# Performance work log

Hardware: AMD Instinct MI355X
Metric: run time of the kernel (lower is better)

Reference implementation:

```python
import jax, jax.numpy as jnp
import numpy as np

N_NODES = 50000
N_EDGES = 800000
DIM = 256


def setup_inputs() -> dict:
    key = jax.random.key(0)
    k1, k2, k3, k4 = jax.random.split(key, 4)
    x = jax.random.normal(k1, (N_NODES, DIM), dtype=jnp.float32)
    edge_index = jax.random.randint(k2, (2, N_EDGES), 0, N_NODES, dtype=jnp.int64)
    # GCNConv learned params (glorot-style weight, zero bias like PyG default init)
    W = jax.random.normal(k3, (DIM, DIM), dtype=jnp.float32) * (1.0 / np.sqrt(DIM))
    b = jnp.zeros((DIM,), dtype=jnp.float32)
    return {"x": x, "edge_index": edge_index, "W": W, "b": b}


def reference(x, edge_index, W, b):
    # GNNBlock forward (eval mode: dropout is identity; normalizer=Identity,
    # activation=ReLU, projection=Identity since in_dim==out_dim).
    n = x.shape[0]
    # --- GCNConv with self-loops and symmetric normalization ---
    loop = jnp.arange(n, dtype=edge_index.dtype)
    src = jnp.concatenate([edge_index[0], loop])  # [E+N]
    dst = jnp.concatenate([edge_index[1], loop])  # [E+N]
    ones = jnp.ones(src.shape[0], dtype=x.dtype)
    deg = jax.ops.segment_sum(ones, dst, num_segments=n)  # in-degree incl. self-loop
    dinv = jnp.where(deg > 0, jax.lax.rsqrt(deg), 0.0)
    norm = dinv[src] * dinv[dst]  # [E+N]
    h = x @ W  # transform first (in->out), then aggregate
    msg = h[src] * norm[:, None]  # gather + scale, [E+N, DIM]
    agg = jax.ops.segment_sum(msg, dst, num_segments=n) + b  # scatter-add
    # --- norm (Identity) -> activation (ReLU) -> residual -> dropout (eval) ---
    out = jax.nn.relu(agg) + x
    return out
```

## Files before the change

kernel.cpp:

```cpp
#include <hip/hip_runtime.h>

#define N_NODES 50000
#define DIM 256
#define NBUCK 196
#define BCAP 6144
#define CEDGES 2048
#define APAD 264
#define EPAD 260

typedef __attribute__((ext_vector_type(8))) short bf16x8;
typedef __attribute__((ext_vector_type(4))) float f32x4;
typedef __attribute__((ext_vector_type(2))) float f32x2;
union U16 { uint4 u; bf16x8 s; };

__device__ __forceinline__ unsigned short f2b(float f) {
    unsigned int u = __float_as_uint(f);
    return (unsigned short)((u + 0x7FFFu + ((u >> 16) & 1u)) >> 16);
}

__global__ __launch_bounds__(256) void coarse_kernel(const int* __restrict__ src,
                                                     const int* __restrict__ dst, int E,
                                                     int* __restrict__ bcur,
                                                     unsigned int* __restrict__ slab) {
    __shared__ int hist[NBUCK];
    __shared__ int scn[NBUCK];
    __shared__ int gbase[NBUCK];
    __shared__ int cur[NBUCK];
    __shared__ int s2[256];
    __shared__ unsigned int sorted[CEDGES];

    const int tid = threadIdx.x;
    const int e0 = blockIdx.x * CEDGES;
    const int nE = min(CEDGES, E - e0);

    if (tid < NBUCK) hist[tid] = 0;
    __syncthreads();

    unsigned int pk[8];
    #pragma unroll
    for (int i = 0; i < 8; ++i) {
        int idx = i * 256 + tid;
        pk[i] = 0xFFFFFFFFu;
        if (idx < nE) {
            unsigned int s = (unsigned int)src[e0 + idx];
            unsigned int d = (unsigned int)dst[e0 + idx];
            pk[i] = (d << 16) | s;
            atomicAdd(&hist[d >> 8], 1);
        }
    }
    __syncthreads();

    int v = (tid < NBUCK) ? hist[tid] : 0;
    s2[tid] = v;
    __syncthreads();
    for (int off = 1; off < 256; off <<= 1) {
        int t = (tid >= off) ? s2[tid - off] : 0;
        __syncthreads();
        s2[tid] += t;
        __syncthreads();
    }
    if (tid < NBUCK) {
        scn[tid] = s2[tid] - v;
        cur[tid] = 0;
        gbase[tid] = (v > 0) ? atomicAdd(&bcur[tid], v) : 0;
    }
    __syncthreads();

    #pragma unroll
    for (int i = 0; i < 8; ++i) {
        if (pk[i] != 0xFFFFFFFFu) {
            int bkt = pk[i] >> 24;
            int p = scn[bkt] + atomicAdd(&cur[bkt], 1);
            sorted[p] = pk[i];
        }
    }
    __syncthreads();

    for (int i = tid; i < nE; i += 256) {
        unsigned int p = sorted[i];
        int bkt = p >> 24;
        int gpos = gbase[bkt] + (i - scn[bkt]);
        if (gpos < BCAP) slab[(size_t)bkt * BCAP + gpos] = p;
    }
}

__global__ __launch_bounds__(256) void fine_kernel(const int* __restrict__ bcnt,
                                                   const unsigned int* __restrict__ slab,
                                                   int* __restrict__ offs,
                                                   int* __restrict__ deg,
                                                   float* __restrict__ dinv,
                                                   int* __restrict__ csr_src) {
    __shared__ int red[256];
    __shared__ int hist[256];
    __shared__ int scn[256];
    __shared__ unsigned int stage[BCAP];

    const int tid = threadIdx.x;
    const int g = blockIdx.x;

    red[tid] = (tid < g) ? min(bcnt[tid], BCAP) : 0;
    __syncthreads();
    for (int off = 128; off > 0; off >>= 1) {
        if (tid < off) red[tid] += red[tid + off];
        __syncthreads();
    }
    const int base = red[0];
    const int cnt = min(bcnt[g], BCAP);

    hist[tid] = 0;
    __syncthreads();
    for (int i = tid; i < cnt; i += 256) {
        unsigned int p = slab[(size_t)g * BCAP + i];
        stage[i] = p;
        atomicAdd(&hist[(p >> 16) & 255], 1);
    }
    __syncthreads();

    int d = hist[tid];
    scn[tid] = d;
    __syncthreads();
    for (int off = 1; off < 256; off <<= 1) {
        int t = (tid >= off) ? scn[tid - off] : 0;
        __syncthreads();
        scn[tid] += t;
        __syncthreads();
    }
    int excl = scn[tid] - d;

    int node = g * 256 + tid;
    if (node < N_NODES) {
        offs[node] = base + excl;
        deg[node]  = d;
        dinv[node] = rsqrtf((float)(d + 1));
    }
    hist[tid] = excl;
    __syncthreads();

    for (int i = tid; i < cnt; i += 256) {
        unsigned int p = stage[i];
        int pos = atomicAdd(&hist[(p >> 16) & 255], 1);
        csr_src[base + pos] = (int)(p & 0xFFFFu);
    }
}

__global__ __launch_bounds__(256) void prep_kernel(const float* __restrict__ W,
                                                   uint4* __restrict__ Bpack,
                                                   const float* __restrict__ x,
                                                   const float* __restrict__ dinv,
                                                   unsigned int* __restrict__ xq) {
    if (blockIdx.x < 32) {
        int gid  = blockIdx.x * 256 + threadIdx.x;
        int lane = gid & 63;
        int u    = (gid >> 6) & 15;
        int ki   = gid >> 10;
        int n    = u * 16 + (lane & 15);
        int k0   = ki * 32 + (lane >> 4) * 8;
        unsigned int w[4];
        #pragma unroll
        for (int p = 0; p < 4; ++p) {
            unsigned int lo = f2b(W[(size_t)(k0 + 2 * p) * DIM + n]);
            unsigned int hi = f2b(W[(size_t)(k0 + 2 * p + 1) * DIM + n]);
            w[p] = lo | (hi << 16);
        }
        Bpack[gid] = make_uint4(w[0], w[1], w[2], w[3]);
    } else {
        int gid = (blockIdx.x - 32) * 256 + threadIdx.x;
        int row = gid >> 6;
        float di = dinv[row];
        float4 v = ((const float4*)x)[gid];
        int p = __builtin_amdgcn_cvt_pk_fp8_f32(v.x * di, v.y * di, 0, false);
        p     = __builtin_amdgcn_cvt_pk_fp8_f32(v.z * di, v.w * di, p, true);
        xq[gid] = (unsigned int)p;
    }
}

__global__ __launch_bounds__(256) void agg_q_kernel(const unsigned int* __restrict__ xq,
                                                    const int* __restrict__ offs,
                                                    const int* __restrict__ deg,
                                                    const int* __restrict__ csr_src,
                                                    const float* __restrict__ dinv,
                                                    ushort4* __restrict__ aggb) {
    int row  = blockIdx.x * 4 + (threadIdx.x >> 6);
    int lane = threadIdx.x & 63;
    if (row >= N_NODES) return;

    float di = dinv[row];
    unsigned int qself = xq[(size_t)row * 64 + lane];
    f32x2 lo = __builtin_amdgcn_cvt_pk_f32_fp8((int)qself, false);
    f32x2 hi = __builtin_amdgcn_cvt_pk_f32_fp8((int)qself, true);
    float ax = lo.x, ay = lo.y, az = hi.x, aw = hi.y;

    int start = offs[row];
    int n     = deg[row];
    int i = 0;
    for (; i + 8 <= n; i += 8) {
        int s0 = csr_src[start + i + 0], s1 = csr_src[start + i + 1];
        int s2 = csr_src[start + i + 2], s3 = csr_src[start + i + 3];
        int s4 = csr_src[start + i + 4], s5 = csr_src[start + i + 5];
        int s6 = csr_src[start + i + 6], s7 = csr_src[start + i + 7];
        unsigned int q0 = xq[(size_t)s0 * 64 + lane];
        unsigned int q1 = xq[(size_t)s1 * 64 + lane];
        unsigned int q2 = xq[(size_t)s2 * 64 + lane];
        unsigned int q3 = xq[(size_t)s3 * 64 + lane];
        unsigned int q4 = xq[(size_t)s4 * 64 + lane];
        unsigned int q5 = xq[(size_t)s5 * 64 + lane];
        unsigned int q6 = xq[(size_t)s6 * 64 + lane];
        unsigned int q7 = xq[(size_t)s7 * 64 + lane];
        #pragma unroll
        for (int u = 0; u < 8; ++u) {
            unsigned int q;
            switch (u) {
                case 0: q = q0; break; case 1: q = q1; break;
                case 2: q = q2; break; case 3: q = q3; break;
                case 4: q = q4; break; case 5: q = q5; break;
                case 6: q = q6; break; default: q = q7; break;
            }
            f32x2 l = __builtin_amdgcn_cvt_pk_f32_fp8((int)q, false);
            f32x2 h = __builtin_amdgcn_cvt_pk_f32_fp8((int)q, true);
            ax += l.x; ay += l.y; az += h.x; aw += h.y;
        }
    }
    for (; i < n; ++i) {
        int s = csr_src[start + i];
        unsigned int q = xq[(size_t)s * 64 + lane];
        f32x2 l = __builtin_amdgcn_cvt_pk_f32_fp8((int)q, false);
        f32x2 h = __builtin_amdgcn_cvt_pk_f32_fp8((int)q, true);
        ax += l.x; ay += l.y; az += h.x; aw += h.y;
    }
    ax *= di; ay *= di; az *= di; aw *= di;
    aggb[(size_t)row * 64 + lane] = make_ushort4(f2b(ax), f2b(ay), f2b(az), f2b(aw));
}

__global__ __launch_bounds__(256) void gemm_kernel(const uint4* __restrict__ aggb16,
                                                   const float* __restrict__ x,
                                                   const uint4* __restrict__ Bpack,
                                                   const float* __restrict__ b,
                                                   float* __restrict__ out) {
    __shared__ __align__(16) char LDSraw[64 * APAD * 2];
    ushort* ALDS = (ushort*)LDSraw;
    float*  ELDS = (float*)LDSraw;

    const int tid  = threadIdx.x;
    const int row0 = blockIdx.x * 64;

    #pragma unroll
    for (int i = 0; i < 8; ++i) {
        int c = i * 256 + tid;
        int r = c >> 5;
        int q = c & 31;
        int row = row0 + r;
        uint4 v = make_uint4(0, 0, 0, 0);
        if (row < N_NODES) v = aggb16[(size_t)row * 32 + q];
        *(uint4*)&ALDS[r * APAD + q * 8] = v;
    }
    __syncthreads();

    const int wave = tid >> 6;
    const int lane = tid & 63;
    const int m    = lane & 15;
    const int kb   = lane >> 4;

    f32x4 acc[4][4];
    #pragma unroll
    for (int t = 0; t < 4; ++t)
        #pragma unroll
        for (int r = 0; r < 4; ++r) acc[t][r] = (f32x4){0.f, 0.f, 0.f, 0.f};

    const uint4* bp = Bpack + (size_t)(wave * 4) * 64 + lane;

    for (int ki = 0; ki < 8; ++ki) {
        U16 bf[4], af[4];
        #pragma unroll
        for (int t = 0; t < 4; ++t) bf[t].u = bp[(size_t)(ki * 16 + t) * 64];
        #pragma unroll
        for (int r = 0; r < 4; ++r)
            af[r].u = *(const uint4*)&ALDS[(r * 16 + m) * APAD + ki * 32 + kb * 8];
        #pragma unroll
        for (int t = 0; t < 4; ++t)
            #pragma unroll
            for (int r = 0; r < 4; ++r)
                acc[t][r] = __builtin_amdgcn_mfma_f32_16x16x32_bf16(af[r].s, bf[t].s, acc[t][r], 0, 0, 0);
    }

    const float4* x4g = (const float4*)x;
    const float4* b4  = (const float4*)b;
    float4* out4 = (float4*)out;

    #pragma unroll
    for (int p = 0; p < 2; ++p) {
        __syncthreads();
        #pragma unroll
        for (int t = 0; t < 4; ++t) {
            #pragma unroll
            for (int rl = 0; rl < 2; ++rl) {
                int r = p * 2 + rl;
                #pragma unroll
                for (int reg = 0; reg < 4; ++reg) {
                    ELDS[(rl * 16 + kb * 4 + reg) * EPAD + wave * 64 + t * 16 + m] = acc[t][r][reg];
                }
            }
        }
        __syncthreads();
        #pragma unroll
        for (int j = 0; j < 8; ++j) {
            int idx  = j * 256 + tid;
            int lrow = idx >> 6;
            int c4   = idx & 63;
            int grow = row0 + p * 32 + lrow;
            if (grow < N_NODES) {
                float4 v  = *(const float4*)&ELDS[lrow * EPAD + c4 * 4];
                float4 bb = b4[c4];
                float4 xx = x4g[(size_t)grow * 64 + c4];
                float4 o;
                o.x = fmaxf(v.x + bb.x, 0.f) + xx.x;
                o.y = fmaxf(v.y + bb.y, 0.f) + xx.y;
                o.z = fmaxf(v.z + bb.z, 0.f) + xx.z;
                o.w = fmaxf(v.w + bb.w, 0.f) + xx.w;
                out4[(size_t)grow * 64 + c4] = o;
            }
        }
    }
}

extern "C" void kernel_launch(void* const* d_in, const int* in_sizes, int n_in,
                              void* d_out, int out_size, void* d_ws, size_t ws_size,
                              hipStream_t stream) {
    const float* x  = (const float*)d_in[0];
    const int*   ei = (const int*)d_in[1];
    const float* W  = (const float*)d_in[2];
    const float* b  = (const float*)d_in[3];
    float* out = (float*)d_out;
    const int E = in_sizes[1] / 2;

    char* ws = (char*)d_ws;
    int*          bcur    = (int*)(ws);
    int*          deg     = (int*)(ws + 4096);
    int*          offs    = (int*)(ws + 208896);
    float*        dinv    = (float*)(ws + 413696);
    int*          csr_src = (int*)(ws + 618496);
    unsigned int* slab    = (unsigned int*)(ws + 3821568);
    ushort4*      aggb    = (ushort4*)(ws + 8640512);
    uint4*        Bpack   = (uint4*)(ws + 34240512);
    unsigned int* xq      = (unsigned int*)(ws + 34371584);

    const int* src = ei;
    const int* dst = ei + E;

    hipMemsetAsync(bcur, 0, NBUCK * sizeof(int), stream);

    coarse_kernel<<<(E + CEDGES - 1) / CEDGES, 256, 0, stream>>>(src, dst, E, bcur, slab);
    fine_kernel<<<NBUCK, 256, 0, stream>>>(bcur, slab, offs, deg, dinv, csr_src);
    prep_kernel<<<12532, 256, 0, stream>>>(W, Bpack, x, dinv, xq);
    agg_q_kernel<<<(N_NODES + 3) / 4, 256, 0, stream>>>(xq, offs, deg, csr_src, dinv, aggb);
    gemm_kernel<<<(N_NODES + 63) / 64, 256, 0, stream>>>((const uint4*)aggb, x, Bpack, b, out);
}
```

Baseline: 200.8 us.

## Replace two-pass bucket sort CSR build with cooperative atomic counting-sort kernel

Replaces the coarse/fine bucketed sort that built the CSR with a single cooperative kernel. It does a global atomic degree histogram, a grid-synced block scan for offsets, then scatters source indices through per-node atomic cursors. This removes one launch and the slab staging buffer. In exchange it adds three grid-wide syncs, heavy global atomic contention, and non-deterministic neighbour order within each node's list.

```diff
diff --git a/kernel.cpp b/kernel.cpp
--- a/kernel.cpp
+++ b/kernel.cpp
@@ -1,10 +1,12 @@
 #include <hip/hip_runtime.h>
+#include <hip/hip_cooperative_groups.h>
+
+namespace cg = cooperative_groups;
 
 #define N_NODES 50000
 #define DIM 256
-#define NBUCK 196
-#define BCAP 6144
-#define CEDGES 2048
+#define NBLK 256
+#define CHUNK 196
 #define APAD 264
 #define EPAD 260
 
@@ -18,106 +20,31 @@
     return (unsigned short)((u + 0x7FFFu + ((u >> 16) & 1u)) >> 16);
 }
 
-__global__ __launch_bounds__(256) void coarse_kernel(const int* __restrict__ src,
-                                                     const int* __restrict__ dst, int E,
-                                                     int* __restrict__ bcur,
-                                                     unsigned int* __restrict__ slab) {
-    __shared__ int hist[NBUCK];
-    __shared__ int scn[NBUCK];
-    __shared__ int gbase[NBUCK];
-    __shared__ int cur[NBUCK];
-    __shared__ int s2[256];
-    __shared__ unsigned int sorted[CEDGES];
+__global__ __launch_bounds__(256) void bin_kernel(const int* __restrict__ src,
+                                                  const int* __restrict__ dst, const int E,
+                                                  int* __restrict__ deg,
+                                                  int* __restrict__ offs,
+                                                  int* __restrict__ cursor,
+                                                  float* __restrict__ dinv,
+                                                  int* __restrict__ csr_src,
+                                                  int* __restrict__ bsum) {
+    cg::grid_group grid = cg::this_grid();
+    __shared__ int scn[256];
+    __shared__ int lexcl[256];
 
     const int tid = threadIdx.x;
-    const int e0 = blockIdx.x * CEDGES;
-    const int nE = min(CEDGES, E - e0);
-
-    if (tid < NBUCK) hist[tid] = 0;
-    __syncthreads();
-
-    unsigned int pk[8];
-    #pragma unroll
-    for (int i = 0; i < 8; ++i) {
-        int idx = i * 256 + tid;
-        pk[i] = 0xFFFFFFFFu;
-        if (idx < nE) {
-            unsigned int s = (unsigned int)src[e0 + idx];
-            unsigned int d = (unsigned int)dst[e0 + idx];
-            pk[i] = (d << 16) | s;
-            atomicAdd(&hist[d >> 8], 1);
-        }
-    }
-    __syncthreads();
-
-    int v = (tid < NBUCK) ? hist[tid] : 0;
-    s2[tid] = v;
-    __syncthreads();
-    for (int off = 1; off < 256; off <<= 1) {
-        int t = (tid >= off) ? s2[tid - off] : 0;
-        __syncthreads();
-        s2[tid] += t;
-        __syncthreads();
-    }
-    if (tid < NBUCK) {
-        scn[tid] = s2[tid] - v;
-        cur[tid] = 0;
-        gbase[tid] = (v > 0) ? atomicAdd(&bcur[tid], v) : 0;
-    }
-    __syncthreads();
-
-    #pragma unroll
-    for (int i = 0; i < 8; ++i) {
-        if (pk[i] != 0xFFFFFFFFu) {
-            int bkt = pk[i] >> 24;
-            int p = scn[bkt] + atomicAdd(&cur[bkt], 1);
-            sorted[p] = pk[i];
-        }
-    }
-    __syncthreads();
-
-    for (int i = tid; i < nE; i += 256) {
-        unsigned int p = sorted[i];
-        int bkt = p >> 24;
-        int gpos = gbase[bkt] + (i - scn[bkt]);
-        if (gpos < BCAP) slab[(size_t)bkt * BCAP + gpos] = p;
-    }
-}
-
-__global__ __launch_bounds__(256) void fine_kernel(const int* __restrict__ bcnt,
-                                                   const unsigned int* __restrict__ slab,
-                                                   int* __restrict__ offs,
-                                                   int* __restrict__ deg,
-                                                   float* __restrict__ dinv,
-                                                   int* __restrict__ csr_src) {
-    __shared__ int red[256];
-    __shared__ int hist[256];
-    __shared__ int scn[256];
-    __shared__ unsigned int stage[BCAP];
-
-    const int tid = threadIdx.x;
-    const int g = blockIdx.x;
-
-    red[tid] = (tid < g) ? min(bcnt[tid], BCAP) : 0;
-    __syncthreads();
-    for (int off = 128; off > 0; off >>= 1) {
-        if (tid < off) red[tid] += red[tid + off];
-        __syncthreads();
-    }
-    const int base = red[0];
-    const int cnt = min(bcnt[g], BCAP);
-
-    hist[tid] = 0;
-    __syncthreads();
-    for (int i = tid; i < cnt; i += 256) {
-        unsigned int p = slab[(size_t)g * BCAP + i];
-        stage[i] = p;
-        atomicAdd(&hist[(p >> 16) & 255], 1);
-    }
-    __syncthreads();
-
-    int d = hist[tid];
-    scn[tid] = d;
+    const int bid = blockIdx.x;
+    const int gid = bid * 256 + tid;
+    const int gsz = NBLK * 256;
+
+    for (int e = gid; e < E; e += gsz) atomicAdd(&deg[dst[e]], 1);
+    __threadfence();
+    grid.sync();
+
+    const int node = bid * CHUNK + tid;
+    int v = 0;
+    if (tid < CHUNK && node < N_NODES) v = deg[node];
+    scn[tid] = v;
     __syncthreads();
     for (int off = 1; off < 256; off <<= 1) {
         int t = (tid >= off) ? scn[tid - off] : 0;
@@ -125,21 +52,32 @@
         scn[tid] += t;
         __syncthreads();
     }
-    int excl = scn[tid] - d;
-
-    int node = g * 256 + tid;
-    if (node < N_NODES) {
-        offs[node] = base + excl;
-        deg[node]  = d;
-        dinv[node] = rsqrtf((float)(d + 1));
-    }
-    hist[tid] = excl;
+    lexcl[tid] = scn[tid] - v;
+    if (tid == 255) bsum[bid] = scn[255];
+    __threadfence();
+    grid.sync();
+
+    scn[tid] = (tid < bid) ? bsum[tid] : 0;
     __syncthreads();
-
-    for (int i = tid; i < cnt; i += 256) {
-        unsigned int p = stage[i];
-        int pos = atomicAdd(&hist[(p >> 16) & 255], 1);
-        csr_src[base + pos] = (int)(p & 0xFFFFu);
+    for (int off = 128; off > 0; off >>= 1) {
+        if (tid < off) scn[tid] += scn[tid + off];
+        __syncthreads();
+    }
+    const int base = scn[0];
+    if (tid < CHUNK && node < N_NODES) {
+        int o = base + lexcl[tid];
+        offs[node]   = o;
+        cursor[node] = o;
+        dinv[node]   = rsqrtf((float)(v + 1));
+    }
+    __threadfence();
+    grid.sync();
+
+    for (int e = gid; e < E; e += gsz) {
+        int d = dst[e];
+        int s = src[e];
+        int pos = atomicAdd(&cursor[d], 1);
+        csr_src[pos] = s;
     }
 }
 
@@ -333,23 +271,33 @@
     const int E = in_sizes[1] / 2;
 
     char* ws = (char*)d_ws;
-    int*          bcur    = (int*)(ws);
-    int*          deg     = (int*)(ws + 4096);
-    int*          offs    = (int*)(ws + 208896);
-    float*        dinv    = (float*)(ws + 413696);
-    int*          csr_src = (int*)(ws + 618496);
-    unsigned int* slab    = (unsigned int*)(ws + 3821568);
-    ushort4*      aggb    = (ushort4*)(ws + 8640512);
-    uint4*        Bpack   = (uint4*)(ws + 34240512);
-    unsigned int* xq      = (unsigned int*)(ws + 34371584);
+    int*          deg     = (int*)(ws);
+    int*          offs    = (int*)(ws + 200704);
+    int*          cursor  = (int*)(ws + 401408);
+    float*        dinv    = (float*)(ws + 602112);
+    int*          bsum    = (int*)(ws + 802816);
+    int*          csr_src = (int*)(ws + 803840);
+    ushort4*      aggb    = (ushort4*)(ws + 4003840);
+    uint4*        Bpack   = (uint4*)(ws + 29603840);
+    unsigned int* xq      = (unsigned int*)(ws + 29734912);
 
     const int* src = ei;
     const int* dst = ei + E;
 
-    hipMemsetAsync(bcur, 0, NBUCK * sizeof(int), stream);
-
-    coarse_kernel<<<(E + CEDGES - 1) / CEDGES, 256, 0, stream>>>(src, dst, E, bcur, slab);
-    fine_kernel<<<NBUCK, 256, 0, stream>>>(bcur, slab, offs, deg, dinv, csr_src);
+    hipMemsetAsync(deg, 0, N_NODES * sizeof(int), stream);
+
+    {
+        const int* a_src = src;
+        const int* a_dst = dst;
+        int a_E = E;
+        int* a_deg = deg; int* a_offs = offs; int* a_cursor = cursor;
+        float* a_dinv = dinv; int* a_csr = csr_src; int* a_bsum = bsum;
+        void* args[] = {&a_src, &a_dst, &a_E, &a_deg, &a_offs, &a_cursor,
+                        &a_dinv, &a_csr, &a_bsum};
+        hipLaunchCooperativeKernel((void*)bin_kernel, dim3(NBLK), dim3(256),
+                                   args, 0, stream);
+    }
+
     prep_kernel<<<12532, 256, 0, stream>>>(W, Bpack, x, dinv, xq);
     agg_q_kernel<<<(N_NODES + 3) / 4, 256, 0, stream>>>(xq, offs, deg, csr_src, dinv, aggb);
     gemm_kernel<<<(N_NODES + 63) / 64, 256, 0, stream>>>((const uint4*)aggb, x, Bpack, b, out);
```

Result: slower. 411.6 us (+105.0%).

## Fuse aggregation into GEMM kernel and merge prep with edge binning

Applied to the files above, without the earlier changes.

Quantization of x to fp8 no longer depends on dinv, so it now runs in the same launch as the coarse edge-binning kernel, together with the W packing. The per-edge source normalization moves into the gather loop as an extra dinv load per neighbor. The aggregation is fused into the GEMM kernel: each block aggregates its 64 rows straight into LDS, which removes the bf16 aggb round trip through global memory and two launches. In exchange, GEMM blocks now hold only 4 waves doing irregular gathers (782 blocks in place of 12500), which may lower the latency hiding for the random neighbor loads.

```diff
diff --git a/kernel.cpp b/kernel.cpp
--- a/kernel.cpp
+++ b/kernel.cpp
@@ -18,10 +18,15 @@
     return (unsigned short)((u + 0x7FFFu + ((u >> 16) & 1u)) >> 16);
 }
 
-__global__ __launch_bounds__(256) void coarse_kernel(const int* __restrict__ src,
-                                                     const int* __restrict__ dst, int E,
-                                                     int* __restrict__ bcur,
-                                                     unsigned int* __restrict__ slab) {
+__global__ __launch_bounds__(256) void prep_bin_kernel(const int* __restrict__ src,
+                                                       const int* __restrict__ dst, int E,
+                                                       int nCoarse,
+                                                       int* __restrict__ bcur,
+                                                       unsigned int* __restrict__ slab,
+                                                       const float* __restrict__ W,
+                                                       uint4* __restrict__ Bpack,
+                                                       const float* __restrict__ x,
+                                                       unsigned int* __restrict__ xq) {
     __shared__ int hist[NBUCK];
     __shared__ int scn[NBUCK];
     __shared__ int gbase[NBUCK];
@@ -30,6 +35,34 @@
     __shared__ unsigned int sorted[CEDGES];
 
     const int tid = threadIdx.x;
+
+    if (blockIdx.x >= (unsigned)nCoarse) {
+        int role = blockIdx.x - nCoarse;
+        if (role < 32) {
+            int gid  = role * 256 + tid;
+            int lane = gid & 63;
+            int u    = (gid >> 6) & 15;
+            int ki   = gid >> 10;
+            int n    = u * 16 + (lane & 15);
+            int k0   = ki * 32 + (lane >> 4) * 8;
+            unsigned int w[4];
+            #pragma unroll
+            for (int p = 0; p < 4; ++p) {
+                unsigned int lo = f2b(W[(size_t)(k0 + 2 * p) * DIM + n]);
+                unsigned int hi = f2b(W[(size_t)(k0 + 2 * p + 1) * DIM + n]);
+                w[p] = lo | (hi << 16);
+            }
+            Bpack[gid] = make_uint4(w[0], w[1], w[2], w[3]);
+        } else {
+            int gid = (role - 32) * 256 + tid;
+            float4 v = ((const float4*)x)[gid];
+            int p = __builtin_amdgcn_cvt_pk_fp8_f32(v.x, v.y, 0, false);
+            p     = __builtin_amdgcn_cvt_pk_fp8_f32(v.z, v.w, p, true);
+            xq[gid] = (unsigned int)p;
+        }
+        return;
+    }
+
     const int e0 = blockIdx.x * CEDGES;
     const int nE = min(CEDGES, E - e0);
 
@@ -143,122 +176,84 @@
     }
 }
 
-__global__ __launch_bounds__(256) void prep_kernel(const float* __restrict__ W,
-                                                   uint4* __restrict__ Bpack,
-                                                   const float* __restrict__ x,
-                                                   const float* __restrict__ dinv,
-                                                   unsigned int* __restrict__ xq) {
-    if (blockIdx.x < 32) {
-        int gid  = blockIdx.x * 256 + threadIdx.x;
-        int lane = gid & 63;
-        int u    = (gid >> 6) & 15;
-        int ki   = gid >> 10;
-        int n    = u * 16 + (lane & 15);
-        int k0   = ki * 32 + (lane >> 4) * 8;
-        unsigned int w[4];
-        #pragma unroll
-        for (int p = 0; p < 4; ++p) {
-            unsigned int lo = f2b(W[(size_t)(k0 + 2 * p) * DIM + n]);
-            unsigned int hi = f2b(W[(size_t)(k0 + 2 * p + 1) * DIM + n]);
-            w[p] = lo | (hi << 16);
-        }
-        Bpack[gid] = make_uint4(w[0], w[1], w[2], w[3]);
-    } else {
-        int gid = (blockIdx.x - 32) * 256 + threadIdx.x;
-        int row = gid >> 6;
-        float di = dinv[row];
-        float4 v = ((const float4*)x)[gid];
-        int p = __builtin_amdgcn_cvt_pk_fp8_f32(v.x * di, v.y * di, 0, false);
-        p     = __builtin_amdgcn_cvt_pk_fp8_f32(v.z * di, v.w * di, p, true);
-        xq[gid] = (unsigned int)p;
-    }
-}
-
-__global__ __launch_bounds__(256) void agg_q_kernel(const unsigned int* __restrict__ xq,
-                                                    const int* __restrict__ offs,
-                                                    const int* __restrict__ deg,
-                                                    const int* __restrict__ csr_src,
-                                                    const float* __restrict__ dinv,
-                                                    ushort4* __restrict__ aggb) {
-    int row  = blockIdx.x * 4 + (threadIdx.x >> 6);
-    int lane = threadIdx.x & 63;
-    if (row >= N_NODES) return;
-
-    float di = dinv[row];
-    unsigned int qself = xq[(size_t)row * 64 + lane];
-    f32x2 lo = __builtin_amdgcn_cvt_pk_f32_fp8((int)qself, false);
-    f32x2 hi = __builtin_amdgcn_cvt_pk_f32_fp8((int)qself, true);
-    float ax = lo.x, ay = lo.y, az = hi.x, aw = hi.y;
-
-    int start = offs[row];
-    int n     = deg[row];
-    int i = 0;
-    for (; i + 8 <= n; i += 8) {
-        int s0 = csr_src[start + i + 0], s1 = csr_src[start + i + 1];
-        int s2 = csr_src[start + i + 2], s3 = csr_src[start + i + 3];
-        int s4 = csr_src[start + i + 4], s5 = csr_src[start + i + 5];
-        int s6 = csr_src[start + i + 6], s7 = csr_src[start + i + 7];
-        unsigned int q0 = xq[(size_t)s0 * 64 + lane];
-        unsigned int q1 = xq[(size_t)s1 * 64 + lane];
-        unsigned int q2 = xq[(size_t)s2 * 64 + lane];
-        unsigned int q3 = xq[(size_t)s3 * 64 + lane];
-        unsigned int q4 = xq[(size_t)s4 * 64 + lane];
-        unsigned int q5 = xq[(size_t)s5 * 64 + lane];
-        unsigned int q6 = xq[(size_t)s6 * 64 + lane];
-        unsigned int q7 = xq[(size_t)s7 * 64 + lane];
-        #pragma unroll
-        for (int u = 0; u < 8; ++u) {
-            unsigned int q;
-            switch (u) {
-                case 0: q = q0; break; case 1: q = q1; break;
-                case 2: q = q2; break; case 3: q = q3; break;
-                case 4: q = q4; break; case 5: q = q5; break;
-                case 6: q = q6; break; default: q = q7; break;
-            }
-            f32x2 l = __builtin_amdgcn_cvt_pk_f32_fp8((int)q, false);
-            f32x2 h = __builtin_amdgcn_cvt_pk_f32_fp8((int)q, true);
-            ax += l.x; ay += l.y; az += h.x; aw += h.y;
-        }
-    }
-    for (; i < n; ++i) {
-        int s = csr_src[start + i];
-        unsigned int q = xq[(size_t)s * 64 + lane];
-        f32x2 l = __builtin_amdgcn_cvt_pk_f32_fp8((int)q, false);
-        f32x2 h = __builtin_amdgcn_cvt_pk_f32_fp8((int)q, true);
-        ax += l.x; ay += l.y; az += h.x; aw += h.y;
-    }
-    ax *= di; ay *= di; az *= di; aw *= di;
-    aggb[(size_t)row * 64 + lane] = make_ushort4(f2b(ax), f2b(ay), f2b(az), f2b(aw));
-}
-
-__global__ __launch_bounds__(256) void gemm_kernel(const uint4* __restrict__ aggb16,
-                                                   const float* __restrict__ x,
-                                                   const uint4* __restrict__ Bpack,
-                                                   const float* __restrict__ b,
-                                                   float* __restrict__ out) {
+__global__ __launch_bounds__(256) void agg_gemm_kernel(const unsigned int* __restrict__ xq,
+                                                       const int* __restrict__ offs,
+                                                       const int* __restrict__ deg,
+                                                       const int* __restrict__ csr_src,
+                                                       const float* __restrict__ dinv,
+                                                       const float* __restrict__ x,
+                                                       const uint4* __restrict__ Bpack,
+                                                       const float* __restrict__ b,
+                                                       float* __restrict__ out) {
     __shared__ __align__(16) char LDSraw[64 * APAD * 2];
     ushort* ALDS = (ushort*)LDSraw;
     float*  ELDS = (float*)LDSraw;
 
     const int tid  = threadIdx.x;
     const int row0 = blockIdx.x * 64;
-
-    #pragma unroll
-    for (int i = 0; i < 8; ++i) {
-        int c = i * 256 + tid;
-        int r = c >> 5;
-        int q = c & 31;
-        int row = row0 + r;
-        uint4 v = make_uint4(0, 0, 0, 0);
-        if (row < N_NODES) v = aggb16[(size_t)row * 32 + q];
-        *(uint4*)&ALDS[r * APAD + q * 8] = v;
-    }
-    __syncthreads();
-
     const int wave = tid >> 6;
     const int lane = tid & 63;
-    const int m    = lane & 15;
-    const int kb   = lane >> 4;
+
+    for (int rr = 0; rr < 16; ++rr) {
+        const int r   = wave * 16 + rr;
+        const int row = row0 + r;
+        ushort4 st = make_ushort4(0, 0, 0, 0);
+        if (row < N_NODES) {
+            const float di = dinv[row];
+            unsigned int qself = xq[(size_t)row * 64 + lane];
+            f32x2 lo = __builtin_amdgcn_cvt_pk_f32_fp8((int)qself, false);
+            f32x2 hi = __builtin_amdgcn_cvt_pk_f32_fp8((int)qself, true);
+            float ax = lo.x * di, ay = lo.y * di, az = hi.x * di, aw = hi.y * di;
+
+            const int start = offs[row];
+            const int n     = deg[row];
+            int i = 0;
+            for (; i + 8 <= n; i += 8) {
+                int s0 = csr_src[start + i + 0], s1 = csr_src[start + i + 1];
+                int s2 = csr_src[start + i + 2], s3 = csr_src[start + i + 3];
+                int s4 = csr_src[start + i + 4], s5 = csr_src[start + i + 5];
+                int s6 = csr_src[start + i + 6], s7 = csr_src[start + i + 7];
+                unsigned int q0 = xq[(size_t)s0 * 64 + lane];
+                unsigned int q1 = xq[(size_t)s1 * 64 + lane];
+                unsigned int q2 = xq[(size_t)s2 * 64 + lane];
+                unsigned int q3 = xq[(size_t)s3 * 64 + lane];
+                unsigned int q4 = xq[(size_t)s4 * 64 + lane];
+                unsigned int q5 = xq[(size_t)s5 * 64 + lane];
+                unsigned int q6 = xq[(size_t)s6 * 64 + lane];
+                unsigned int q7 = xq[(size_t)s7 * 64 + lane];
+                float d0 = dinv[s0], d1 = dinv[s1], d2 = dinv[s2], d3 = dinv[s3];
+                float d4 = dinv[s4], d5 = dinv[s5], d6 = dinv[s6], d7 = dinv[s7];
+                #pragma unroll
+                for (int u = 0; u < 8; ++u) {
+                    unsigned int q; float dd;
+                    switch (u) {
+                        case 0: q = q0; dd = d0; break; case 1: q = q1; dd = d1; break;
+                        case 2: q = q2; dd = d2; break; case 3: q = q3; dd = d3; break;
+                        case 4: q = q4; dd = d4; break; case 5: q = q5; dd = d5; break;
+                        case 6: q = q6; dd = d6; break; default: q = q7; dd = d7; break;
+                    }
+                    f32x2 l = __builtin_amdgcn_cvt_pk_f32_fp8((int)q, false);
+                    f32x2 h = __builtin_amdgcn_cvt_pk_f32_fp8((int)q, true);
+                    ax += l.x * dd; ay += l.y * dd; az += h.x * dd; aw += h.y * dd;
+                }
+            }
+            for (; i < n; ++i) {
+                int s = csr_src[start + i];
+                unsigned int q = xq[(size_t)s * 64 + lane];
+                float dd = dinv[s];
+                f32x2 l = __builtin_amdgcn_cvt_pk_f32_fp8((int)q, false);
+                f32x2 h = __builtin_amdgcn_cvt_pk_f32_fp8((int)q, true);
+                ax += l.x * dd; ay += l.y * dd; az += h.x * dd; aw += h.y * dd;
+            }
+            ax *= di; ay *= di; az *= di; aw *= di;
+            st = make_ushort4(f2b(ax), f2b(ay), f2b(az), f2b(aw));
+        }
+        *(ushort4*)&ALDS[r * APAD + lane * 4] = st;
+    }
+    __syncthreads();
+
+    const int m  = lane & 15;
+    const int kb = lane >> 4;
 
     f32x4 acc[4][4];
     #pragma unroll
@@ -339,18 +334,19 @@
     float*        dinv    = (float*)(ws + 413696);
     int*          csr_src = (int*)(ws + 618496);
     unsigned int* slab    = (unsigned int*)(ws + 3821568);
-    ushort4*      aggb    = (ushort4*)(ws + 8640512);
-    uint4*        Bpack   = (uint4*)(ws + 34240512);
-    unsigned int* xq      = (unsigned int*)(ws + 34371584);
+    uint4*        Bpack   = (uint4*)(ws + 8640512);
+    unsigned int* xq      = (unsigned int*)(ws + 8771584);
 
     const int* src = ei;
     const int* dst = ei + E;
 
     hipMemsetAsync(bcur, 0, NBUCK * sizeof(int), stream);
 
-    coarse_kernel<<<(E + CEDGES - 1) / CEDGES, 256, 0, stream>>>(src, dst, E, bcur, slab);
+    const int nCoarse = (E + CEDGES - 1) / CEDGES;
+    const int nXq = (N_NODES * 64) / 256;
+    prep_bin_kernel<<<nCoarse + 32 + nXq, 256, 0, stream>>>(src, dst, E, nCoarse,
+                                                            bcur, slab, W, Bpack, x, xq);
     fine_kernel<<<NBUCK, 256, 0, stream>>>(bcur, slab, offs, deg, dinv, csr_src);
-    prep_kernel<<<12532, 256, 0, stream>>>(W, Bpack, x, dinv, xq);
-    agg_q_kernel<<<(N_NODES + 3) / 4, 256, 0, stream>>>(xq, offs, deg, csr_src, dinv, aggb);
-    gemm_kernel<<<(N_NODES + 63) / 64, 256, 0, stream>>>((const uint4*)aggb, x, Bpack, b, out);
-}
+    agg_gemm_kernel<<<(N_NODES + 63) / 64, 256, 0, stream>>>(xq, offs, deg, csr_src,
+                                                             dinv, x, Bpack, b, out);
+}
```

Result: slower. 255.0 us (+27.0%).
